# Kernel tuning notes

Measured on AMD Instinct MI355X. Metric: run time of the kernel, lower is better.

Reference implementation:

```python
import jax, jax.numpy as jnp
import numpy as np

B, C, H, W = 16, 256, 64, 64
DQ = C // 4


def setup_inputs() -> dict:
    key = jax.random.key(0)
    ks = jax.random.split(key, 6)
    scale = 1.0 / np.sqrt(C)
    return {
        "x_query": jax.random.normal(ks[0], (B, C, W, H), jnp.float32),
        "x_key": jax.random.normal(ks[1], (B, C, W, H), jnp.float32),
        "x_value": jax.random.normal(ks[2], (B, C, W, H), jnp.float32),
        "Wq": jax.random.normal(ks[3], (DQ, C), jnp.float32) * scale,
        "bq": jnp.zeros((DQ,), jnp.float32),
        "Wk": jax.random.normal(ks[4], (DQ, C), jnp.float32) * scale,
        "bk": jnp.zeros((DQ,), jnp.float32),
        "Wv": jax.random.normal(ks[5], (C, C), jnp.float32) * scale,
        "bv": jnp.zeros((C,), jnp.float32),
    }


def reference(x_query, x_key, x_value, Wq, bq, Wk, bk, Wv, bv):
    b, c, w, h = x_value.shape
    n = w * h
    # 1x1 convs == per-pixel linear over channels; flatten spatial to n
    q = (jnp.einsum('oc,bcn->bon', Wq, x_query.reshape(b, c, n))
         + bq[None, :, None])            # [b, dq, n]
    k = (jnp.einsum('oc,bcn->bon', Wk, x_key.reshape(b, c, n))
         + bk[None, :, None])            # [b, dq, n]
    v = (jnp.einsum('oc,bcn->bon', Wv, x_value.reshape(b, c, n))
         + bv[None, :, None])            # [b, c, n]
    # energy = Q^T K  (unscaled), softmax over last dim
    energy = jnp.einsum('bdi,bdj->bij', q, k)        # [b, n, n]
    attention = jax.nn.softmax(energy, axis=-1)
    # out = V @ attention : out[b,c,i] = sum_j V[b,c,j] * att[b,j,i]
    out = jnp.einsum('bcj,bji->bci', v, attention)   # [b, c, n]
    return out.reshape(b, c, w, h)
```

## Files before the change

kernel.cpp:

```cpp
#include <hip/hip_runtime.h>
#include <hip/hip_bf16.h>
#include <stddef.h>

#define BATCH 16
#define CH    256
#define NPIX  4096
#define DQH   64
#define L2E   1.44269504088896340736f

typedef __attribute__((ext_vector_type(8))) short bf16x8;
typedef __attribute__((ext_vector_type(4))) float floatx4;

__device__ __forceinline__ unsigned short f2bf(float f) {
  union { float f; unsigned int u; } v; v.f = f;
  unsigned int u = v.u;
  u += 0x7fffu + ((u >> 16) & 1u);
  return (unsigned short)(u >> 16);
}

__device__ __forceinline__ unsigned int pk2bf(float a, float b) {
  __hip_bfloat162 h = __float22bfloat162_rn(float2{a, b});
  union { __hip_bfloat162 h; unsigned int u; } cv;
  cv.h = h;
  return cv.u;
}

__device__ __forceinline__ bf16x8 ldbf8(const unsigned short* p) {
  return *(const bf16x8*)p;
}

__device__ __forceinline__ int xcd_swz(int lin, int nwg) {
  return (lin & 7) * (nwg >> 3) + (lin >> 3);
}

__global__ __launch_bounds__(256) void wconv_kernel(
    const float* __restrict__ Wq, const float* __restrict__ Wk,
    const float* __restrict__ Wv, unsigned short* __restrict__ Wb) {
  const int idx = blockIdx.x * 256 + threadIdx.x;
  float v;
  if (idx < 64 * CH)            v = Wq[idx] * L2E;
  else if (idx < 128 * CH)      v = Wk[idx - 64 * CH];
  else                          v = Wv[idx - 128 * CH];
  Wb[idx] = f2bf(v);
}

__global__ __launch_bounds__(256) void proj_kernel(
    const float* __restrict__ xq, const float* __restrict__ xk,
    const float* __restrict__ xv, const unsigned short* __restrict__ Wb,
    const float* __restrict__ bq, const float* __restrict__ bk,
    const float* __restrict__ bv,
    unsigned short* __restrict__ Qb, unsigned short* __restrict__ Kb,
    unsigned short* __restrict__ Vb) {
  __shared__ __attribute__((aligned(16))) float xtile[32][260];
  const int t    = threadIdx.x;
  const int lane = t & 63;
  const int w    = t >> 6;
  const int l15  = lane & 15;
  const int quad = lane >> 4;
  const int b    = blockIdx.y;
  const int pxbase = blockIdx.x * 256;
  const int z    = blockIdx.z;

  const float* X; const float* bt; int dbase; int wbase;
  if (z == 0)      { X = xq; bt = bq; dbase = 0;            wbase = 0; }
  else if (z == 1) { X = xk; bt = bk; dbase = 0;            wbase = 64; }
  else             { X = xv; bt = bv; dbase = (z - 2) * 64; wbase = 128 + (z - 2) * 64; }

  floatx4 acc[4][4];
#pragma unroll
  for (int mt = 0; mt < 4; ++mt)
#pragma unroll
    for (int nt = 0; nt < 4; ++nt)
      acc[mt][nt] = (floatx4){0.f, 0.f, 0.f, 0.f};

  const int px4 = (t & 63) * 4;
  const float* xbase = X + (size_t)b * CH * NPIX + pxbase + px4;

  for (int kb = 0; kb < 8; ++kb) {
#pragma unroll
    for (int i = 0; i < 8; ++i) {
      const int cloc = w + i * 4;
      const float4 xv4 = *(const float4*)(xbase + (size_t)(kb * 32 + cloc) * NPIX);
      *(float4*)&xtile[cloc][px4] = xv4;
    }
    __syncthreads();

#pragma unroll
    for (int nt = 0; nt < 4; ++nt) {
      const int pxl = w * 64 + nt * 16 + l15;
      float f[8];
#pragma unroll
      for (int j = 0; j < 8; ++j) f[j] = xtile[quad * 8 + j][pxl];
      union { bf16x8 v; unsigned int u[4]; } bb;
      bb.u[0] = pk2bf(f[0], f[1]);
      bb.u[1] = pk2bf(f[2], f[3]);
      bb.u[2] = pk2bf(f[4], f[5]);
      bb.u[3] = pk2bf(f[6], f[7]);
#pragma unroll
      for (int mt = 0; mt < 4; ++mt) {
        const bf16x8 aA =
            ldbf8(Wb + (size_t)(wbase + mt * 16 + l15) * CH + kb * 32 + quad * 8);
        acc[mt][nt] =
            __builtin_amdgcn_mfma_f32_16x16x32_bf16(aA, bb.v, acc[mt][nt], 0, 0, 0);
      }
    }
    __syncthreads();
  }

  float4 bias4[4];
#pragma unroll
  for (int mt = 0; mt < 4; ++mt)
    bias4[mt] = *(const float4*)&bt[dbase + mt * 16 + quad * 4];
  if (z == 0) {
#pragma unroll
    for (int mt = 0; mt < 4; ++mt) {
      bias4[mt].x *= L2E; bias4[mt].y *= L2E;
      bias4[mt].z *= L2E; bias4[mt].w *= L2E;
    }
  }

  if (z >= 2) {
#pragma unroll
    for (int mt = 0; mt < 4; ++mt)
#pragma unroll
      for (int nt = 0; nt < 4; ++nt) {
        const int px = pxbase + w * 64 + nt * 16 + l15;
#pragma unroll
        for (int r = 0; r < 4; ++r) {
          const int c = dbase + mt * 16 + quad * 4 + r;
          Vb[((size_t)b * CH + c) * NPIX + px] =
              f2bf(acc[mt][nt][r] + ((const float*)&bias4[mt])[r]);
        }
      }
  } else {
    unsigned short* Ob = (z == 0) ? Qb : Kb;
#pragma unroll
    for (int mt = 0; mt < 4; ++mt)
#pragma unroll
      for (int nt = 0; nt < 4; ++nt) {
        const int px = pxbase + w * 64 + nt * 16 + l15;
        uint2 qp;
        qp.x = pk2bf(acc[mt][nt][0] + ((const float*)&bias4[mt])[0],
                     acc[mt][nt][1] + ((const float*)&bias4[mt])[1]);
        qp.y = pk2bf(acc[mt][nt][2] + ((const float*)&bias4[mt])[2],
                     acc[mt][nt][3] + ((const float*)&bias4[mt])[3]);
        *(uint2*)&Ob[((size_t)b * NPIX + px) * DQH + mt * 16 + quad * 4] = qp;
      }
  }
}

__global__ __launch_bounds__(256) void pass1_kernel(
    const unsigned short* __restrict__ Qb, const unsigned short* __restrict__ Kb,
    float* __restrict__ Srow) {
  const int t    = threadIdx.x;
  const int lane = t & 63;
  const int w    = t >> 6;
  const int l15  = lane & 15;
  const int quad = lane >> 4;
  const int lin  = blockIdx.x + (blockIdx.y << 6);
  const int swz  = xcd_swz(lin, 64 * BATCH);
  const int b     = swz >> 6;
  const int jbase = (swz & 63) * 64 + w * 16;

  const unsigned short* qrow = Qb + ((size_t)b * NPIX + jbase + l15) * DQH;
  const bf16x8 qA0 = ldbf8(qrow + quad * 8);
  const bf16x8 qA1 = ldbf8(qrow + 32 + quad * 8);

  float lsum[4] = {0.f, 0.f, 0.f, 0.f};

  const unsigned short* kbase = Kb + (size_t)b * NPIX * DQH;
  for (int ib = 0; ib < NPIX; ib += 64) {
#pragma unroll
    for (int nt = 0; nt < 4; ++nt) {
      const unsigned short* krow = kbase + (size_t)(ib + nt * 16 + l15) * DQH;
      const bf16x8 kB0 = ldbf8(krow + quad * 8);
      const bf16x8 kB1 = ldbf8(krow + 32 + quad * 8);
      floatx4 a = {0.f, 0.f, 0.f, 0.f};
      a = __builtin_amdgcn_mfma_f32_16x16x32_bf16(qA0, kB0, a, 0, 0, 0);
      a = __builtin_amdgcn_mfma_f32_16x16x32_bf16(qA1, kB1, a, 0, 0, 0);
#pragma unroll
      for (int r = 0; r < 4; ++r) lsum[r] += exp2f(a[r]);
    }
  }

#pragma unroll
  for (int r = 0; r < 4; ++r) {
    float s = lsum[r];
    s += __shfl_xor(s, 1);
    s += __shfl_xor(s, 2);
    s += __shfl_xor(s, 4);
    s += __shfl_xor(s, 8);
    if (l15 == 0)
      Srow[(size_t)b * NPIX + jbase + quad * 4 + r] = log2f(s);
  }
}

__global__ __launch_bounds__(256, 4) void pass2_kernel(
    const unsigned short* __restrict__ Qb, const unsigned short* __restrict__ Kb,
    const unsigned short* __restrict__ Vb, const float* __restrict__ Srow,
    float* __restrict__ out) {
  __shared__ __attribute__((aligned(16))) unsigned short Plds[2][64][72];
  __shared__ __attribute__((aligned(16))) unsigned short Qlds[2][64][72];
  const int t    = threadIdx.x;
  const int lane = t & 63;
  const int w    = t >> 6;
  const int l15  = lane & 15;
  const int quad = lane >> 4;
  const int lin  = blockIdx.x + (blockIdx.y << 6);
  const int swz  = xcd_swz(lin, 64 * BATCH);
  const int b     = swz >> 6;
  const int ibase = (swz & 63) * 64;

  const unsigned short* krow = Kb + ((size_t)b * NPIX + ibase + w * 16 + l15) * DQH;
  const bf16x8 kB0 = ldbf8(krow + quad * 8);
  const bf16x8 kB1 = ldbf8(krow + 32 + quad * 8);

  floatx4 accO[4][4];
#pragma unroll
  for (int mt = 0; mt < 4; ++mt)
#pragma unroll
    for (int nt = 0; nt < 4; ++nt)
      accO[mt][nt] = (floatx4){0.f, 0.f, 0.f, 0.f};

  const float* sp          = Srow + (size_t)b * NPIX;
  const unsigned short* qb = Qb + (size_t)b * NPIX * DQH;
  const unsigned short* vb = Vb + (size_t)b * CH * NPIX;

  const int srow = t >> 3;
  const int sseg = t & 7;

  {
    const unsigned short* qsrc = qb + (size_t)srow * DQH + sseg * 8;
    *(uint4*)&Qlds[0][srow][sseg * 8]      = *(const uint4*)qsrc;
    *(uint4*)&Qlds[0][srow + 32][sseg * 8] = *(const uint4*)(qsrc + 32 * DQH);
  }
  __syncthreads();

  int cur = 0;
  for (int jb = 0; jb < NPIX; jb += 64) {
    const int jn = (jb + 64) & (NPIX - 1);
    const unsigned short* qsrc = qb + (size_t)(jn + srow) * DQH + sseg * 8;
    const uint4 d0 = *(const uint4*)qsrc;
    const uint4 d1 = *(const uint4*)(qsrc + 32 * DQH);

#pragma unroll
    for (int jt = 0; jt < 4; ++jt) {
      const bf16x8 q0 = ldbf8(&Qlds[cur][jt * 16 + l15][quad * 8]);
      const bf16x8 q1 = ldbf8(&Qlds[cur][jt * 16 + l15][32 + quad * 8]);
      floatx4 a = {0.f, 0.f, 0.f, 0.f};
      a = __builtin_amdgcn_mfma_f32_16x16x32_bf16(q0, kB0, a, 0, 0, 0);
      a = __builtin_amdgcn_mfma_f32_16x16x32_bf16(q1, kB1, a, 0, 0, 0);
      const float4 s4 = *(const float4*)&sp[jb + jt * 16 + quad * 4];
      uint2 pk;
      pk.x = pk2bf(exp2f(a[0] - s4.x), exp2f(a[1] - s4.y));
      pk.y = pk2bf(exp2f(a[2] - s4.z), exp2f(a[3] - s4.w));
      *(uint2*)&Plds[cur][w * 16 + l15][jt * 16 + quad * 4] = pk;
    }

    *(uint4*)&Qlds[cur ^ 1][srow][sseg * 8]      = d0;
    *(uint4*)&Qlds[cur ^ 1][srow + 32][sseg * 8] = d1;

    __syncthreads();

#pragma unroll
    for (int ks = 0; ks < 2; ++ks) {
      bf16x8 pB[4];
#pragma unroll
      for (int nt = 0; nt < 4; ++nt)
        pB[nt] = ldbf8(&Plds[cur][nt * 16 + l15][ks * 32 + quad * 8]);
#pragma unroll
      for (int mt = 0; mt < 4; ++mt) {
        const unsigned short* vrow =
            vb + (size_t)(w * 64 + mt * 16 + l15) * NPIX + jb + ks * 32;
        const bf16x8 vA = ldbf8(vrow + quad * 8);
#pragma unroll
        for (int nt = 0; nt < 4; ++nt)
          accO[mt][nt] =
              __builtin_amdgcn_mfma_f32_16x16x32_bf16(vA, pB[nt], accO[mt][nt], 0, 0, 0);
      }
    }
    cur ^= 1;
  }

#pragma unroll
  for (int mt = 0; mt < 4; ++mt) {
#pragma unroll
    for (int nt = 0; nt < 4; ++nt) {
#pragma unroll
      for (int r = 0; r < 4; ++r) {
        const int c = w * 64 + mt * 16 + quad * 4 + r;
        const int i = ibase + nt * 16 + l15;
        out[((size_t)b * CH + c) * NPIX + i] = accO[mt][nt][r];
      }
    }
  }
}

extern "C" void kernel_launch(void* const* d_in, const int* in_sizes, int n_in,
                              void* d_out, int out_size, void* d_ws, size_t ws_size,
                              hipStream_t stream) {
  (void)in_sizes; (void)n_in; (void)out_size; (void)ws_size;
  const float* xq = (const float*)d_in[0];
  const float* xk = (const float*)d_in[1];
  const float* xv = (const float*)d_in[2];
  const float* Wq = (const float*)d_in[3];
  const float* bq = (const float*)d_in[4];
  const float* Wk = (const float*)d_in[5];
  const float* bk = (const float*)d_in[6];
  const float* Wv = (const float*)d_in[7];
  const float* bv = (const float*)d_in[8];
  float* out = (float*)d_out;

  char* ws = (char*)d_ws;
  const size_t qk_bytes = (size_t)BATCH * NPIX * DQH * 2;
  const size_t v_bytes  = (size_t)BATCH * CH * NPIX * 2;
  const size_t s_bytes  = (size_t)BATCH * NPIX * 4;
  unsigned short* Qb = (unsigned short*)(ws);
  unsigned short* Kb = (unsigned short*)(ws + qk_bytes);
  unsigned short* Vb = (unsigned short*)(ws + 2 * qk_bytes);
  float* Srow        = (float*)(ws + 2 * qk_bytes + v_bytes);
  unsigned short* Wb = (unsigned short*)(ws + 2 * qk_bytes + v_bytes + s_bytes);

  wconv_kernel<<<dim3(384), 256, 0, stream>>>(Wq, Wk, Wv, Wb);
  proj_kernel<<<dim3(16, 16, 6), 256, 0, stream>>>(xq, xk, xv, Wb, bq, bk, bv,
                                                   Qb, Kb, Vb);
  pass1_kernel<<<dim3(64, 16), 256, 0, stream>>>(Qb, Kb, Srow);
  pass2_kernel<<<dim3(64, 16), 256, 0, stream>>>(Qb, Kb, Vb, Srow, out);
}
```

Baseline: 755.7 us.

## Prefetch global loads into registers and swizzle LDS tile across kernels

The projection kernel now loads the next channel block of X into registers while the current block is staged in shared memory. Its LDS tile drops the padding and uses an XOR-style column rotation to avoid bank conflicts instead. Pass1 double-buffers K fragments in registers so the next tile's loads overlap the current MFMAs and exp2. Pass2 issues the V fragment and row-sum loads at the top of each iteration, before the QK^T/softmax phase, and raises wave priority around the PV MFMA block. These changes hide global memory latency at the cost of extra registers, which may reduce occupancy in pass2 under launch_bounds(256,4).

```diff
diff --git a/kernel.cpp b/kernel.cpp
--- a/kernel.cpp
+++ b/kernel.cpp
@@ -51,7 +51,7 @@
     const float* __restrict__ bv,
     unsigned short* __restrict__ Qb, unsigned short* __restrict__ Kb,
     unsigned short* __restrict__ Vb) {
-  __shared__ __attribute__((aligned(16))) float xtile[32][260];
+  __shared__ __attribute__((aligned(16))) float xtile[32][256];
   const int t    = threadIdx.x;
   const int lane = t & 63;
   const int w    = t >> 6;
@@ -76,21 +76,32 @@
   const int px4 = (t & 63) * 4;
   const float* xbase = X + (size_t)b * CH * NPIX + pxbase + px4;
 
+  float4 xr[8], xrN[8];
+#pragma unroll
+  for (int i = 0; i < 8; ++i)
+    xr[i] = *(const float4*)(xbase + (size_t)(w + i * 4) * NPIX);
+
   for (int kb = 0; kb < 8; ++kb) {
 #pragma unroll
     for (int i = 0; i < 8; ++i) {
       const int cloc = w + i * 4;
-      const float4 xv4 = *(const float4*)(xbase + (size_t)(kb * 32 + cloc) * NPIX);
-      *(float4*)&xtile[cloc][px4] = xv4;
+      const int cpx  = (px4 + ((cloc >> 3) << 3)) & 255;
+      *(float4*)&xtile[cloc][cpx] = xr[i];
+    }
+    if (kb < 7) {
+#pragma unroll
+      for (int i = 0; i < 8; ++i)
+        xrN[i] = *(const float4*)(xbase + (size_t)((kb + 1) * 32 + w + i * 4) * NPIX);
     }
     __syncthreads();
 
 #pragma unroll
     for (int nt = 0; nt < 4; ++nt) {
       const int pxl = w * 64 + nt * 16 + l15;
+      const int pxr = (pxl + (quad << 3)) & 255;
       float f[8];
 #pragma unroll
-      for (int j = 0; j < 8; ++j) f[j] = xtile[quad * 8 + j][pxl];
+      for (int j = 0; j < 8; ++j) f[j] = xtile[quad * 8 + j][pxr];
       union { bf16x8 v; unsigned int u[4]; } bb;
       bb.u[0] = pk2bf(f[0], f[1]);
       bb.u[1] = pk2bf(f[2], f[3]);
@@ -105,6 +116,8 @@
       }
     }
     __syncthreads();
+#pragma unroll
+    for (int i = 0; i < 8; ++i) xr[i] = xrN[i];
   }
 
   float4 bias4[4];
@@ -169,17 +182,35 @@
   float lsum[4] = {0.f, 0.f, 0.f, 0.f};
 
   const unsigned short* kbase = Kb + (size_t)b * NPIX * DQH;
+
+  bf16x8 kC[4][2], kN[4][2];
+#pragma unroll
+  for (int nt = 0; nt < 4; ++nt) {
+    const unsigned short* krow = kbase + (size_t)(nt * 16 + l15) * DQH;
+    kC[nt][0] = ldbf8(krow + quad * 8);
+    kC[nt][1] = ldbf8(krow + 32 + quad * 8);
+  }
+
   for (int ib = 0; ib < NPIX; ib += 64) {
-#pragma unroll
-    for (int nt = 0; nt < 4; ++nt) {
-      const unsigned short* krow = kbase + (size_t)(ib + nt * 16 + l15) * DQH;
-      const bf16x8 kB0 = ldbf8(krow + quad * 8);
-      const bf16x8 kB1 = ldbf8(krow + 32 + quad * 8);
+    const int in = (ib + 64) & (NPIX - 1);
+#pragma unroll
+    for (int nt = 0; nt < 4; ++nt) {
+      const unsigned short* krow = kbase + (size_t)(in + nt * 16 + l15) * DQH;
+      kN[nt][0] = ldbf8(krow + quad * 8);
+      kN[nt][1] = ldbf8(krow + 32 + quad * 8);
+    }
+#pragma unroll
+    for (int nt = 0; nt < 4; ++nt) {
       floatx4 a = {0.f, 0.f, 0.f, 0.f};
-      a = __builtin_amdgcn_mfma_f32_16x16x32_bf16(qA0, kB0, a, 0, 0, 0);
-      a = __builtin_amdgcn_mfma_f32_16x16x32_bf16(qA1, kB1, a, 0, 0, 0);
+      a = __builtin_amdgcn_mfma_f32_16x16x32_bf16(qA0, kC[nt][0], a, 0, 0, 0);
+      a = __builtin_amdgcn_mfma_f32_16x16x32_bf16(qA1, kC[nt][1], a, 0, 0, 0);
 #pragma unroll
       for (int r = 0; r < 4; ++r) lsum[r] += exp2f(a[r]);
+    }
+#pragma unroll
+    for (int nt = 0; nt < 4; ++nt) {
+      kC[nt][0] = kN[nt][0];
+      kC[nt][1] = kN[nt][1];
     }
   }
 
@@ -238,6 +269,19 @@
 
   int cur = 0;
   for (int jb = 0; jb < NPIX; jb += 64) {
+    bf16x8 vF[2][4];
+#pragma unroll
+    for (int ks = 0; ks < 2; ++ks)
+#pragma unroll
+      for (int mt = 0; mt < 4; ++mt)
+        vF[ks][mt] = ldbf8(vb + (size_t)(w * 64 + mt * 16 + l15) * NPIX
+                           + jb + ks * 32 + quad * 8);
+
+    float4 s4[4];
+#pragma unroll
+    for (int jt = 0; jt < 4; ++jt)
+      s4[jt] = *(const float4*)&sp[jb + jt * 16 + quad * 4];
+
     const int jn = (jb + 64) & (NPIX - 1);
     const unsigned short* qsrc = qb + (size_t)(jn + srow) * DQH + sseg * 8;
     const uint4 d0 = *(const uint4*)qsrc;
@@ -250,10 +294,9 @@
       floatx4 a = {0.f, 0.f, 0.f, 0.f};
       a = __builtin_amdgcn_mfma_f32_16x16x32_bf16(q0, kB0, a, 0, 0, 0);
       a = __builtin_amdgcn_mfma_f32_16x16x32_bf16(q1, kB1, a, 0, 0, 0);
-      const float4 s4 = *(const float4*)&sp[jb + jt * 16 + quad * 4];
       uint2 pk;
-      pk.x = pk2bf(exp2f(a[0] - s4.x), exp2f(a[1] - s4.y));
-      pk.y = pk2bf(exp2f(a[2] - s4.z), exp2f(a[3] - s4.w));
+      pk.x = pk2bf(exp2f(a[0] - s4[jt].x), exp2f(a[1] - s4[jt].y));
+      pk.y = pk2bf(exp2f(a[2] - s4[jt].z), exp2f(a[3] - s4[jt].w));
       *(uint2*)&Plds[cur][w * 16 + l15][jt * 16 + quad * 4] = pk;
     }
 
@@ -262,6 +305,7 @@
 
     __syncthreads();
 
+    __builtin_amdgcn_s_setprio(1);
 #pragma unroll
     for (int ks = 0; ks < 2; ++ks) {
       bf16x8 pB[4];
@@ -269,16 +313,13 @@
       for (int nt = 0; nt < 4; ++nt)
         pB[nt] = ldbf8(&Plds[cur][nt * 16 + l15][ks * 32 + quad * 8]);
 #pragma unroll
-      for (int mt = 0; mt < 4; ++mt) {
-        const unsigned short* vrow =
-            vb + (size_t)(w * 64 + mt * 16 + l15) * NPIX + jb + ks * 32;
-        const bf16x8 vA = ldbf8(vrow + quad * 8);
+      for (int mt = 0; mt < 4; ++mt)
 #pragma unroll
         for (int nt = 0; nt < 4; ++nt)
-          accO[mt][nt] =
-              __builtin_amdgcn_mfma_f32_16x16x32_bf16(vA, pB[nt], accO[mt][nt], 0, 0, 0);
-      }
-    }
+          accO[mt][nt] = __builtin_amdgcn_mfma_f32_16x16x32_bf16(
+              vF[ks][mt], pB[nt], accO[mt][nt], 0, 0, 0);
+    }
+    __builtin_amdgcn_s_setprio(0);
     cur ^= 1;
   }
 
```

Result: slower. 1.302 ms (+72.3%).

## Use direct global-to-LDS loads in projection and prefetch K in row-sum pass

Applied to the files above, without the earlier changes.

The projection kernel now loads input tiles straight into LDS with global_load_lds, removing the register staging step. It drops the padded row stride and uses a per-row rotation swizzle instead to avoid bank conflicts. The pass-1 row-sum kernel double-buffers K fragments in registers, loading the next 64-row block while computing MFMAs and exp2 on the current one, to hide global load latency. This costs more registers in pass1 and adds address arithmetic for the swizzle. The last iteration prefetches a block that wraps around and is never used.

```diff
diff --git a/kernel.cpp b/kernel.cpp
--- a/kernel.cpp
+++ b/kernel.cpp
@@ -31,6 +31,12 @@
 
 __device__ __forceinline__ int xcd_swz(int lin, int nwg) {
   return (lin & 7) * (nwg >> 3) + (lin >> 3);
+}
+
+__device__ __forceinline__ void gload_lds16(const void* g, void* l) {
+  __builtin_amdgcn_global_load_lds(
+      (const __attribute__((address_space(1))) void*)g,
+      (__attribute__((address_space(3))) void*)l, 16, 0, 0);
 }
 
 __global__ __launch_bounds__(256) void wconv_kernel(
@@ -51,7 +57,7 @@
     const float* __restrict__ bv,
     unsigned short* __restrict__ Qb, unsigned short* __restrict__ Kb,
     unsigned short* __restrict__ Vb) {
-  __shared__ __attribute__((aligned(16))) float xtile[32][260];
+  __shared__ __attribute__((aligned(16))) float xtile[32][256];
   const int t    = threadIdx.x;
   const int lane = t & 63;
   const int w    = t >> 6;
@@ -73,15 +79,16 @@
     for (int nt = 0; nt < 4; ++nt)
       acc[mt][nt] = (floatx4){0.f, 0.f, 0.f, 0.f};
 
-  const int px4 = (t & 63) * 4;
-  const float* xbase = X + (size_t)b * CH * NPIX + pxbase + px4;
+  const float* xb0 = X + (size_t)b * CH * NPIX + pxbase;
 
   for (int kb = 0; kb < 8; ++kb) {
 #pragma unroll
     for (int i = 0; i < 8; ++i) {
       const int cloc = w + i * 4;
-      const float4 xv4 = *(const float4*)(xbase + (size_t)(kb * 32 + cloc) * NPIX);
-      *(float4*)&xtile[cloc][px4] = xv4;
+      const int rot  = (cloc >> 3) << 3;
+      const int colf = ((lane << 2) - rot) & 255;
+      gload_lds16(xb0 + (size_t)(kb * 32 + cloc) * NPIX + colf,
+                  &xtile[cloc][0]);
     }
     __syncthreads();
 
@@ -90,7 +97,10 @@
       const int pxl = w * 64 + nt * 16 + l15;
       float f[8];
 #pragma unroll
-      for (int j = 0; j < 8; ++j) f[j] = xtile[quad * 8 + j][pxl];
+      for (int j = 0; j < 8; ++j) {
+        const int row = quad * 8 + j;
+        f[j] = xtile[row][(pxl + ((row >> 3) << 3)) & 255];
+      }
       union { bf16x8 v; unsigned int u[4]; } bb;
       bb.u[0] = pk2bf(f[0], f[1]);
       bb.u[1] = pk2bf(f[2], f[3]);
@@ -169,17 +179,35 @@
   float lsum[4] = {0.f, 0.f, 0.f, 0.f};
 
   const unsigned short* kbase = Kb + (size_t)b * NPIX * DQH;
+
+  bf16x8 kC[4][2], kN[4][2];
+#pragma unroll
+  for (int nt = 0; nt < 4; ++nt) {
+    const unsigned short* krow = kbase + (size_t)(nt * 16 + l15) * DQH;
+    kC[nt][0] = ldbf8(krow + quad * 8);
+    kC[nt][1] = ldbf8(krow + 32 + quad * 8);
+  }
+
   for (int ib = 0; ib < NPIX; ib += 64) {
-#pragma unroll
-    for (int nt = 0; nt < 4; ++nt) {
-      const unsigned short* krow = kbase + (size_t)(ib + nt * 16 + l15) * DQH;
-      const bf16x8 kB0 = ldbf8(krow + quad * 8);
-      const bf16x8 kB1 = ldbf8(krow + 32 + quad * 8);
+    const int in = (ib + 64) & (NPIX - 1);
+#pragma unroll
+    for (int nt = 0; nt < 4; ++nt) {
+      const unsigned short* krow = kbase + (size_t)(in + nt * 16 + l15) * DQH;
+      kN[nt][0] = ldbf8(krow + quad * 8);
+      kN[nt][1] = ldbf8(krow + 32 + quad * 8);
+    }
+#pragma unroll
+    for (int nt = 0; nt < 4; ++nt) {
       floatx4 a = {0.f, 0.f, 0.f, 0.f};
-      a = __builtin_amdgcn_mfma_f32_16x16x32_bf16(qA0, kB0, a, 0, 0, 0);
-      a = __builtin_amdgcn_mfma_f32_16x16x32_bf16(qA1, kB1, a, 0, 0, 0);
+      a = __builtin_amdgcn_mfma_f32_16x16x32_bf16(qA0, kC[nt][0], a, 0, 0, 0);
+      a = __builtin_amdgcn_mfma_f32_16x16x32_bf16(qA1, kC[nt][1], a, 0, 0, 0);
 #pragma unroll
       for (int r = 0; r < 4; ++r) lsum[r] += exp2f(a[r]);
+    }
+#pragma unroll
+    for (int nt = 0; nt < 4; ++nt) {
+      kC[nt][0] = kN[nt][0];
+      kC[nt][1] = kN[nt][1];
     }
   }
 
```

New measurement: 755.8 us. About the same (+0.0%).
